# Performance work log

Measured on AMD Instinct MI355X. Metric: run time of the kernel, lower is better.

## Reference

```python
import jax, jax.numpy as jnp
import numpy as np


def setup_inputs() -> dict:
    key = jax.random.key(0)
    ks = jax.random.split(key, 11)
    B, D, H = 2048, 1024, 1024
    return {
        "x": jax.random.normal(ks[0], (B, D), jnp.float32),
        "h_prev": jax.random.normal(ks[1], (B, H), jnp.float32),
        "W_mu": jax.random.normal(ks[2], (D, 3 * H), jnp.float32) * 0.05,
        "W_rho": jax.random.normal(ks[3], (D, 3 * H), jnp.float32) - 4.0,
        "U_mu": jax.random.normal(ks[4], (H, 3 * H), jnp.float32) * 0.05,
        "U_rho": jax.random.normal(ks[5], (H, 3 * H), jnp.float32) - 4.0,
        "b_mu": jax.random.normal(ks[6], (3 * H,), jnp.float32) * 0.05,
        "b_rho": jax.random.normal(ks[7], (3 * H,), jnp.float32) - 4.0,
        "r_eps": jax.random.normal(ks[8], (H,), jnp.float32),
        "u_eps": jax.random.normal(ks[9], (H,), jnp.float32),
        "h_pre_eps": jax.random.normal(ks[10], (H,), jnp.float32),
    }


def reference(x, h_prev, W_mu, W_rho, U_mu, U_rho, b_mu, b_rho,
              r_eps, u_eps, h_pre_eps):
    # Local reparameterization GRU cell (Bayes-by-Backprop).
    # Fused mean path: [B, 3H]
    mu = x @ W_mu + h_prev @ U_mu + b_mu
    # Variance path: E[x]^2 with sigma = softplus(rho); note original adds
    # b_sig (not squared) as in the source code.
    W_sig2 = jnp.square(jax.nn.softplus(W_rho))
    U_sig2 = jnp.square(jax.nn.softplus(U_rho))
    b_sig = jax.nn.softplus(b_rho)
    sig = jnp.square(x) @ W_sig2 + jnp.square(h_prev) @ U_sig2 + b_sig

    H = h_prev.shape[1]
    mu_r, mu_u, mu_h = mu[:, :H], mu[:, H:2 * H], mu[:, 2 * H:]
    sig_r, sig_u, sig_h = sig[:, :H], sig[:, H:2 * H], sig[:, 2 * H:]

    r = jax.nn.sigmoid(mu_r + sig_r * r_eps)  # computed as in source (unused in local path h update)
    u = jax.nn.sigmoid(mu_u + sig_u * u_eps)
    h_pre = jnp.tanh(mu_h + sig_h * h_pre_eps)
    h = u * h_prev + (1.0 - u) * h_pre
    return h
```

## Files before the change

kernel.cpp:

```cpp
#include <hip/hip_runtime.h>
#include <stdint.h>

#define BB 2048
#define DD 1024
#define HH 1024
#define KK 4096
#define NN 2048

typedef __bf16 bf16x8 __attribute__((ext_vector_type(8)));
typedef float  f32x4  __attribute__((ext_vector_type(4)));
typedef unsigned short u16x8 __attribute__((ext_vector_type(8)));

__device__ __forceinline__ unsigned short f2bf(float f) {
  union { float f; uint32_t u; } v; v.f = f;
  uint32_t r = (v.u + 0x7FFFu + ((v.u >> 16) & 1u)) >> 16;
  return (unsigned short)r;
}
__device__ __forceinline__ float bf2f(unsigned short u) {
  union { float f; uint32_t i; } v; v.i = ((uint32_t)u) << 16; return v.f;
}

__device__ __forceinline__ float softplus_f(float x) {
  return (x > 20.f) ? x : __logf(1.f + __expf(x));
}

__global__ __launch_bounds__(256) void prep_aw(const float* __restrict__ x,
                                               const float* __restrict__ h,
                                               unsigned short* __restrict__ A,
                                               const float* __restrict__ Wmu,
                                               const float* __restrict__ Wrho,
                                               const float* __restrict__ Umu,
                                               const float* __restrict__ Urho,
                                               const float* __restrict__ ueps,
                                               const float* __restrict__ heps,
                                               unsigned short* __restrict__ Wt) {
  __shared__ float tile[64][65];
  int bxx = blockIdx.x;
  if (bxx >= 2048) {
    int T = (bxx - 2048) * 256 + threadIdx.x;
    int m  = T >> 10;
    int k4 = (T & 1023) << 2;
    int region = k4 >> 10;
    int off = k4 & 1023;
    const float* src = (region & 1) ? h : x;
    float4 v = *(const float4*)(src + (size_t)m * 1024 + off);
    if (region >= 2) { v.x *= v.x; v.y *= v.y; v.z *= v.z; v.w *= v.w; }
    ushort4 o;
    o.x = f2bf(v.x); o.y = f2bf(v.y); o.z = f2bf(v.z); o.w = f2bf(v.w);
    *(ushort4*)(A + (size_t)m * KK + k4) = o;
    return;
  }
  int bx = bxx;
  int n0 = (bx & 31) * 64;
  int k0 = (bx >> 5) * 64;
  int t = threadIdx.x;

  const float* src; int rowbase; bool sig = (k0 >= 2048);
  if      (k0 < 1024) { src = Wmu;  rowbase = k0; }
  else if (k0 < 2048) { src = Umu;  rowbase = k0 - 1024; }
  else if (k0 < 3072) { src = Wrho; rowbase = k0 - 2048; }
  else                { src = Urho; rowbase = k0 - 3072; }

  int nn  = t & 63;
  int kk0 = t >> 6;
  int n   = n0 + nn;
  float eps = 0.f;
  if (sig) eps = (n < 1024) ? ueps[n] : heps[n - 1024];
#pragma unroll
  for (int p = 0; p < 16; ++p) {
    int kk = p * 4 + kk0;
    float v = src[(size_t)(rowbase + kk) * 3072 + 1024 + n];
    if (sig) { float s = softplus_f(v); v = s * s * eps; }
    tile[kk][nn] = v;
  }
  __syncthreads();
#pragma unroll
  for (int p = 0; p < 2; ++p) {
    int idx = p * 256 + t;
    int nw  = idx >> 3;
    int oc  = idx & 7;
    u16x8 o8;
#pragma unroll
    for (int e = 0; e < 8; ++e) o8[e] = f2bf(tile[oc * 8 + e][nw]);
    *(u16x8*)&Wt[(size_t)(n0 + nw) * KK + k0 + oc * 8] = o8;
  }
}

__device__ __forceinline__ void gload16(const unsigned short* g, unsigned short* l) {
  __builtin_amdgcn_global_load_lds((const __attribute__((address_space(1))) void*)g,
                                   (__attribute__((address_space(3))) void*)l, 16, 0, 0);
}

#define BAR() { asm volatile("" ::: "memory"); __builtin_amdgcn_s_barrier(); \
                asm volatile("" ::: "memory"); }
#define WAITL() { asm volatile("s_waitcnt lgkmcnt(0)" ::: "memory"); \
                  __builtin_amdgcn_sched_barrier(0); }
#define VMC(N) { asm volatile("s_waitcnt vmcnt(" #N ")" ::: "memory"); }

template <int SPLITK>
__global__ __launch_bounds__(512, 4) void gemm256(const unsigned short* __restrict__ A,
                                                  const unsigned short* __restrict__ Bt,
                                                  unsigned short* __restrict__ Gb) {
  constexpr int KSTEPS = (KK / 32) / SPLITK;
  static_assert(KSTEPS >= 4, "");
  __shared__ __align__(16) unsigned short lds[36864];
  const int tid = threadIdx.x;
  const int bx  = blockIdx.x;
  const int tile = bx & 127;
  const int kz   = bx >> 7;
  const int m0 = (tile >> 3) * 128;
  const int n0 = (tile & 7) * 256;
  const int kt0 = kz * KSTEPS;
  const int lane = tid & 63;
  const int wid  = tid >> 6;
  const int wm  = wid >> 2;
  const int wn  = wid & 3;
  const int lr  = lane & 15;
  const int lk  = lane >> 4;
  const int roct = lk ^ (lr & 3);

  f32x4 acc[4][4];
#pragma unroll
  for (int i = 0; i < 4; ++i)
#pragma unroll
    for (int j = 0; j < 4; ++j) acc[i][j] = (f32x4)0.f;

#define STAGE3(tl, sbuf) do { if ((tl) < KSTEPS) {                             \
    {                                                                          \
      int c = tid;                                                \
      int row = c >> 2, oc = (c & 3) ^ (row & 3);                              \
      gload16(A + (size_t)(m0 + row) * KK + (size_t)(kt0 + (tl)) * 32 + oc * 8,\
              &lds[(sbuf) * 12288 + c * 8]);                                   \
    }                                                                          \
    _Pragma("unroll") for (int j = 0; j < 2; ++j) {                            \
      int cb = j * 512 + tid;                                     \
      int row = cb >> 2, oc = (cb & 3) ^ (row & 3);                            \
      gload16(Bt + (size_t)(n0 + row) * KK + (size_t)(kt0 + (tl)) * 32 + oc * 8,\
              &lds[(sbuf) * 12288 + 4096 + cb * 8]);                           \
    } } } while (0)

  STAGE3(0, 0);
  STAGE3(1, 1);
  VMC(3); BAR();

  int bufc = 0, sb = 2;
#pragma unroll 1
  for (int tc = 0; tc < KSTEPS; ++tc) {
    bf16x8 a[4], b[4];
#pragma unroll
    for (int f = 0; f < 4; ++f) {
      int row = wm * 64 + f * 16 + lr;
      a[f] = *(const bf16x8*)&lds[bufc * 12288 + row * 32 + roct * 8];
    }
#pragma unroll
    for (int f = 0; f < 4; ++f) {
      int row = wn * 64 + f * 16 + lr;
      b[f] = *(const bf16x8*)&lds[bufc * 12288 + 4096 + row * 32 + roct * 8];
    }
    STAGE3(tc + 2, sb);
    BAR(); WAITL();
    __builtin_amdgcn_s_setprio(1);
#pragma unroll
    for (int fi = 0; fi < 4; ++fi)
#pragma unroll
      for (int fj = 0; fj < 4; ++fj)
        acc[fi][fj] = __builtin_amdgcn_mfma_f32_16x16x32_bf16(a[fi], b[fj],
                                                              acc[fi][fj], 0, 0, 0);
    __builtin_amdgcn_s_setprio(0);
    if (tc + 3 <= KSTEPS) { VMC(3); } else { VMC(0); }
    BAR();
    bufc = (bufc == 2) ? 0 : bufc + 1;
    sb   = (sb   == 2) ? 0 : sb   + 1;
  }

  unsigned short* wl = &lds[wid * 4096];
#pragma unroll
  for (int fi = 0; fi < 4; ++fi)
#pragma unroll
    for (int fj = 0; fj < 4; ++fj) {
#pragma unroll
      for (int q = 0; q < 4; ++q) {
        int row = fi * 16 + lk * 4 + q;
        int col = fj * 16 + lr;
        int oct = (col >> 3) ^ (row & 7);
        wl[row * 64 + oct * 8 + (col & 7)] = f2bf(acc[fi][fj][q]);
      }
    }
  unsigned short* Gz = Gb + (size_t)kz * BB * NN;
  {
    const int rl = lane >> 3;
    const int c8 = lane & 7;
#pragma unroll
    for (int i = 0; i < 8; ++i) {
      int r = i * 8 + rl;
      bf16x8 vv = *(const bf16x8*)&wl[r * 64 + ((c8 ^ (r & 7)) * 8)];
      *(bf16x8*)&Gz[(size_t)(m0 + wm * 64 + r) * NN + n0 + wn * 64 + c8 * 8] = vv;
    }
  }
#undef STAGE3
}

template <int SPLITK>
__global__ __launch_bounds__(256) void epilogue(const unsigned short* __restrict__ Gb,
                                                const float* __restrict__ hprev,
                                                const float* __restrict__ bmu,
                                                const float* __restrict__ brho,
                                                const float* __restrict__ ueps,
                                                const float* __restrict__ heps,
                                                float* __restrict__ out) {
  int T = blockIdx.x * 256 + threadIdx.x;
  int m  = T >> 7;
  int j8 = (T & 127) << 3;
  float gu[8] = {0.f,0.f,0.f,0.f,0.f,0.f,0.f,0.f};
  float gh[8] = {0.f,0.f,0.f,0.f,0.f,0.f,0.f,0.f};
#pragma unroll
  for (int z = 0; z < SPLITK; ++z) {
    const unsigned short* Gz = Gb + (size_t)z * BB * NN;
    u16x8 a = *(const u16x8*)(Gz + (size_t)m * NN + j8);
    u16x8 c = *(const u16x8*)(Gz + (size_t)m * NN + 1024 + j8);
#pragma unroll
    for (int e = 0; e < 8; ++e) { gu[e] += bf2f(a[e]); gh[e] += bf2f(c[e]); }
  }
  float hp[8], bu[8], ru[8], bh[8], rh[8], ue[8], he[8];
  *(float4*)&hp[0] = *(const float4*)(hprev + (size_t)m * 1024 + j8);
  *(float4*)&hp[4] = *(const float4*)(hprev + (size_t)m * 1024 + j8 + 4);
  *(float4*)&bu[0] = *(const float4*)(bmu + 1024 + j8);
  *(float4*)&bu[4] = *(const float4*)(bmu + 1024 + j8 + 4);
  *(float4*)&ru[0] = *(const float4*)(brho + 1024 + j8);
  *(float4*)&ru[4] = *(const float4*)(brho + 1024 + j8 + 4);
  *(float4*)&bh[0] = *(const float4*)(bmu + 2048 + j8);
  *(float4*)&bh[4] = *(const float4*)(bmu + 2048 + j8 + 4);
  *(float4*)&rh[0] = *(const float4*)(brho + 2048 + j8);
  *(float4*)&rh[4] = *(const float4*)(brho + 2048 + j8 + 4);
  *(float4*)&ue[0] = *(const float4*)(ueps + j8);
  *(float4*)&ue[4] = *(const float4*)(ueps + j8 + 4);
  *(float4*)&he[0] = *(const float4*)(heps + j8);
  *(float4*)&he[4] = *(const float4*)(heps + j8 + 4);
  float o[8];
#pragma unroll
  for (int c = 0; c < 8; ++c) {
    float zu = gu[c] + bu[c] + softplus_f(ru[c]) * ue[c];
    float zh = gh[c] + bh[c] + softplus_f(rh[c]) * he[c];
    float u  = 1.f / (1.f + __expf(-zu));
    float e2 = __expf(2.f * zh);
    float th = 1.f - 2.f / (e2 + 1.f);
    o[c] = u * hp[c] + (1.f - u) * th;
  }
  *(float4*)(out + (size_t)m * 1024 + j8)     = *(const float4*)&o[0];
  *(float4*)(out + (size_t)m * 1024 + j8 + 4) = *(const float4*)&o[4];
}

extern "C" void kernel_launch(void* const* d_in, const int* in_sizes, int n_in,
                              void* d_out, int out_size, void* d_ws, size_t ws_size,
                              hipStream_t stream) {
  const float* x     = (const float*)d_in[0];
  const float* hprev = (const float*)d_in[1];
  const float* Wmu   = (const float*)d_in[2];
  const float* Wrho  = (const float*)d_in[3];
  const float* Umu   = (const float*)d_in[4];
  const float* Urho  = (const float*)d_in[5];
  const float* bmu   = (const float*)d_in[6];
  const float* brho  = (const float*)d_in[7];
  const float* ueps  = (const float*)d_in[9];
  const float* heps  = (const float*)d_in[10];
  float* out = (float*)d_out;

  size_t aw = (size_t)BB * KK * 2;
  size_t ww = (size_t)NN * KK * 2;
  size_t gw = (size_t)BB * NN * 2;
  unsigned short* Abf = (unsigned short*)d_ws;
  unsigned short* Wt  = (unsigned short*)((char*)d_ws + aw);
  unsigned short* Gb  = (unsigned short*)((char*)d_ws + aw + ww);

  int splitk = 1;
  if      (ws_size >= aw + ww + 4 * gw) splitk = 4;
  else if (ws_size >= aw + ww + 2 * gw) splitk = 2;

  prep_aw<<<10240, 256, 0, stream>>>(x, hprev, Abf, Wmu, Wrho, Umu, Urho,
                                     ueps, heps, Wt);
  if (splitk == 4) {
    gemm256<4><<<512, 512, 0, stream>>>(Abf, Wt, Gb);
    epilogue<4><<<1024, 256, 0, stream>>>(Gb, hprev, bmu, brho, ueps, heps, out);
  } else if (splitk == 2) {
    gemm256<2><<<256, 512, 0, stream>>>(Abf, Wt, Gb);
    epilogue<2><<<1024, 256, 0, stream>>>(Gb, hprev, bmu, brho, ueps, heps, out);
  } else {
    gemm256<1><<<128, 512, 0, stream>>>(Abf, Wt, Gb);
    epilogue<1><<<1024, 256, 0, stream>>>(Gb, hprev, bmu, brho, ueps, heps, out);
  }
}
```

Before: 73.18 us.

## Replace 128x256 8-wave GEMM with 256x256 4-wave tile, BK=64 double buffering

Measured after the change: 73.40 us. No clear change (+0.3%).

```diff
diff --git a/kernel.cpp b/kernel.cpp
--- a/kernel.cpp
+++ b/kernel.cpp
@@ -93,111 +93,111 @@
 
 #define BAR() { asm volatile("" ::: "memory"); __builtin_amdgcn_s_barrier(); \
                 asm volatile("" ::: "memory"); }
-#define WAITL() { asm volatile("s_waitcnt lgkmcnt(0)" ::: "memory"); \
-                  __builtin_amdgcn_sched_barrier(0); }
 #define VMC(N) { asm volatile("s_waitcnt vmcnt(" #N ")" ::: "memory"); }
 
 template <int SPLITK>
-__global__ __launch_bounds__(512, 4) void gemm256(const unsigned short* __restrict__ A,
-                                                  const unsigned short* __restrict__ Bt,
-                                                  unsigned short* __restrict__ Gb) {
-  constexpr int KSTEPS = (KK / 32) / SPLITK;
-  static_assert(KSTEPS >= 4, "");
-  __shared__ __align__(16) unsigned short lds[36864];
+__global__ __launch_bounds__(256, 1) void gemm4w(const unsigned short* __restrict__ A,
+                                                 const unsigned short* __restrict__ Bt,
+                                                 unsigned short* __restrict__ Gb) {
+  constexpr int KSTEPS = (KK / 64) / SPLITK;
+  __shared__ __align__(16) unsigned short lds[65536];
   const int tid = threadIdx.x;
   const int bx  = blockIdx.x;
-  const int tile = bx & 127;
-  const int kz   = bx >> 7;
-  const int m0 = (tile >> 3) * 128;
+  const int tile = bx & 63;
+  const int kz   = bx >> 6;
+  const int m0 = (tile >> 3) * 256;
   const int n0 = (tile & 7) * 256;
   const int kt0 = kz * KSTEPS;
   const int lane = tid & 63;
   const int wid  = tid >> 6;
-  const int wm  = wid >> 2;
-  const int wn  = wid & 3;
+  const int wr  = wid >> 1;
+  const int wc  = wid & 1;
   const int lr  = lane & 15;
   const int lk  = lane >> 4;
-  const int roct = lk ^ (lr & 3);
-
-  f32x4 acc[4][4];
-#pragma unroll
-  for (int i = 0; i < 4; ++i)
-#pragma unroll
-    for (int j = 0; j < 4; ++j) acc[i][j] = (f32x4)0.f;
-
-#define STAGE3(tl, sbuf) do { if ((tl) < KSTEPS) {                             \
-    {                                                                          \
-      int c = tid;                                                \
-      int row = c >> 2, oc = (c & 3) ^ (row & 3);                              \
-      gload16(A + (size_t)(m0 + row) * KK + (size_t)(kt0 + (tl)) * 32 + oc * 8,\
-              &lds[(sbuf) * 12288 + c * 8]);                                   \
+  const int swz = lr & 7;
+
+  f32x4 acc[8][8];
+#pragma unroll
+  for (int i = 0; i < 8; ++i)
+#pragma unroll
+    for (int j = 0; j < 8; ++j) acc[i][j] = (f32x4)0.f;
+
+#define STG(tl) do { if ((tl) < KSTEPS) {                                      \
+    unsigned short* lb = &lds[((tl) & 1) * 32768];                             \
+    _Pragma("unroll") for (int j = 0; j < 8; ++j) {                            \
+      int c = j * 256 + tid; int row = c >> 3; int oc = (c & 7) ^ (row & 7);   \
+      gload16(A + (size_t)(m0 + row) * KK + (size_t)(kt0 + (tl)) * 64 + oc * 8,\
+              lb + c * 8);                                                     \
     }                                                                          \
-    _Pragma("unroll") for (int j = 0; j < 2; ++j) {                            \
-      int cb = j * 512 + tid;                                     \
-      int row = cb >> 2, oc = (cb & 3) ^ (row & 3);                            \
-      gload16(Bt + (size_t)(n0 + row) * KK + (size_t)(kt0 + (tl)) * 32 + oc * 8,\
-              &lds[(sbuf) * 12288 + 4096 + cb * 8]);                           \
+    _Pragma("unroll") for (int j = 0; j < 8; ++j) {                            \
+      int c = j * 256 + tid; int row = c >> 3; int oc = (c & 7) ^ (row & 7);   \
+      gload16(Bt + (size_t)(n0 + row) * KK + (size_t)(kt0 + (tl)) * 64 + oc * 8,\
+              lb + 16384 + c * 8);                                             \
     } } } while (0)
 
-  STAGE3(0, 0);
-  STAGE3(1, 1);
-  VMC(3); BAR();
-
-  int bufc = 0, sb = 2;
+  STG(0);
+  VMC(0); BAR();
+
 #pragma unroll 1
   for (int tc = 0; tc < KSTEPS; ++tc) {
-    bf16x8 a[4], b[4];
-#pragma unroll
-    for (int f = 0; f < 4; ++f) {
-      int row = wm * 64 + f * 16 + lr;
-      a[f] = *(const bf16x8*)&lds[bufc * 12288 + row * 32 + roct * 8];
+    const unsigned short* lb = &lds[(tc & 1) * 32768];
+    STG(tc + 1);
+    bf16x8 b[8][2];
+#pragma unroll
+    for (int fj = 0; fj < 8; ++fj)
+#pragma unroll
+      for (int ks = 0; ks < 2; ++ks) {
+        int row = wc * 128 + fj * 16 + lr;
+        b[fj][ks] = *(const bf16x8*)&lb[16384 + row * 64 + ((ks * 4 + lk) ^ swz) * 8];
+      }
+#pragma unroll
+    for (int q = 0; q < 4; ++q) {
+      bf16x8 a2[2][2];
+#pragma unroll
+      for (int f2 = 0; f2 < 2; ++f2)
+#pragma unroll
+        for (int ks = 0; ks < 2; ++ks) {
+          int row = wr * 128 + q * 32 + f2 * 16 + lr;
+          a2[f2][ks] = *(const bf16x8*)&lb[row * 64 + ((ks * 4 + lk) ^ swz) * 8];
+        }
+      __builtin_amdgcn_s_setprio(1);
+#pragma unroll
+      for (int ks = 0; ks < 2; ++ks)
+#pragma unroll
+        for (int f2 = 0; f2 < 2; ++f2)
+#pragma unroll
+          for (int fj = 0; fj < 8; ++fj)
+            acc[q * 2 + f2][fj] = __builtin_amdgcn_mfma_f32_16x16x32_bf16(
+                a2[f2][ks], b[fj][ks], acc[q * 2 + f2][fj], 0, 0, 0);
+      __builtin_amdgcn_s_setprio(0);
     }
-#pragma unroll
-    for (int f = 0; f < 4; ++f) {
-      int row = wn * 64 + f * 16 + lr;
-      b[f] = *(const bf16x8*)&lds[bufc * 12288 + 4096 + row * 32 + roct * 8];
-    }
-    STAGE3(tc + 2, sb);
-    BAR(); WAITL();
-    __builtin_amdgcn_s_setprio(1);
-#pragma unroll
-    for (int fi = 0; fi < 4; ++fi)
-#pragma unroll
-      for (int fj = 0; fj < 4; ++fj)
-        acc[fi][fj] = __builtin_amdgcn_mfma_f32_16x16x32_bf16(a[fi], b[fj],
-                                                              acc[fi][fj], 0, 0, 0);
-    __builtin_amdgcn_s_setprio(0);
-    if (tc + 3 <= KSTEPS) { VMC(3); } else { VMC(0); }
-    BAR();
-    bufc = (bufc == 2) ? 0 : bufc + 1;
-    sb   = (sb   == 2) ? 0 : sb   + 1;
-  }
-
-  unsigned short* wl = &lds[wid * 4096];
-#pragma unroll
-  for (int fi = 0; fi < 4; ++fi)
-#pragma unroll
-    for (int fj = 0; fj < 4; ++fj) {
+    VMC(0); BAR();
+  }
+
+  unsigned short* wl = &lds[wid * 16384];
+#pragma unroll
+  for (int fi = 0; fi < 8; ++fi)
+#pragma unroll
+    for (int fj = 0; fj < 8; ++fj) {
 #pragma unroll
       for (int q = 0; q < 4; ++q) {
         int row = fi * 16 + lk * 4 + q;
         int col = fj * 16 + lr;
-        int oct = (col >> 3) ^ (row & 7);
-        wl[row * 64 + oct * 8 + (col & 7)] = f2bf(acc[fi][fj][q]);
+        int oc  = (col >> 3) ^ (row & 7);
+        wl[row * 128 + oc * 8 + (col & 7)] = f2bf(acc[fi][fj][q]);
       }
     }
+  __syncthreads();
   unsigned short* Gz = Gb + (size_t)kz * BB * NN;
-  {
-    const int rl = lane >> 3;
-    const int c8 = lane & 7;
-#pragma unroll
-    for (int i = 0; i < 8; ++i) {
-      int r = i * 8 + rl;
-      bf16x8 vv = *(const bf16x8*)&wl[r * 64 + ((c8 ^ (r & 7)) * 8)];
-      *(bf16x8*)&Gz[(size_t)(m0 + wm * 64 + r) * NN + n0 + wn * 64 + c8 * 8] = vv;
-    }
-  }
-#undef STAGE3
+#pragma unroll
+  for (int i = 0; i < 32; ++i) {
+    int idx = i * 64 + lane;
+    int r   = idx >> 4;
+    int oc  = idx & 15;
+    bf16x8 vv = *(const bf16x8*)&wl[r * 128 + (oc ^ (r & 7)) * 8];
+    *(bf16x8*)&Gz[(size_t)(m0 + wr * 128 + r) * NN + n0 + wc * 128 + oc * 8] = vv;
+  }
+#undef STG
 }
 
 template <int SPLITK>
@@ -279,13 +279,13 @@
   prep_aw<<<10240, 256, 0, stream>>>(x, hprev, Abf, Wmu, Wrho, Umu, Urho,
                                      ueps, heps, Wt);
   if (splitk == 4) {
-    gemm256<4><<<512, 512, 0, stream>>>(Abf, Wt, Gb);
+    gemm4w<4><<<256, 256, 0, stream>>>(Abf, Wt, Gb);
     epilogue<4><<<1024, 256, 0, stream>>>(Gb, hprev, bmu, brho, ueps, heps, out);
   } else if (splitk == 2) {
-    gemm256<2><<<256, 512, 0, stream>>>(Abf, Wt, Gb);
+    gemm4w<2><<<128, 256, 0, stream>>>(Abf, Wt, Gb);
     epilogue<2><<<1024, 256, 0, stream>>>(Gb, hprev, bmu, brho, ueps, heps, out);
   } else {
-    gemm256<1><<<128, 512, 0, stream>>>(Abf, Wt, Gb);
+    gemm4w<1><<<64, 256, 0, stream>>>(Abf, Wt, Gb);
     epilogue<1><<<1024, 256, 0, stream>>>(Gb, hprev, bmu, brho, ueps, heps, out);
   }
 }
```
